# Kernel optimization log

Hardware: AMD Instinct MI355X
Metric: run time of the kernel (lower is better)

## Reference

```python
import jax, jax.numpy as jnp
import numpy as np

ALPHA = 0.2  # LeakyReLU negative slope (init arg `alpha`)
N, F_IN, F_OUT = 8192, 512, 256


def setup_inputs() -> dict:
    key = jax.random.key(0)
    k1, k2, k3, k4 = jax.random.split(key, 4)
    x = jax.random.normal(k1, (N, F_IN), dtype=jnp.float32)
    adj = jax.random.randint(k2, (N, N), 0, 2, dtype=jnp.int32)
    W = jax.random.normal(k3, (F_IN, F_OUT), dtype=jnp.float32) * (1.0 / np.sqrt(F_IN))
    a = jax.random.normal(k4, (2 * F_OUT, 1), dtype=jnp.float32) * (1.0 / np.sqrt(F_IN))
    return {"x": x, "adj": adj, "W": W, "a": a}


def reference(x, adj, W, a):
    h = x @ W  # [N, F_OUT]
    f_out = W.shape[1]
    # e[i,j] = LeakyReLU(a1 . h_i + a2 . h_j); computed without the O(N^2*2F) concat
    f1 = h @ a[:f_out, 0]   # [N]
    f2 = h @ a[f_out:, 0]   # [N]
    s = f1[:, None] + f2[None, :]  # [N, N]
    e = jnp.where(s >= 0, s, ALPHA * s)
    # Faithful to the source bug: -9e15 * zeros_like == zeros, so masked entries are 0.0
    att = jnp.where(adj > 0, e, jnp.zeros((), dtype=e.dtype))
    att = jax.nn.softmax(att, axis=1)
    # dropout is identity in eval mode
    h_prime = att @ h  # [N, F_OUT]
    return jax.nn.elu(h_prime)  # concat=True branch
```

## Files before the change

### kernel.cpp

```cpp
#include <hip/hip_runtime.h>
#include <stdint.h>

#define NN 8192
#define FIN 512
#define FOUT 256
#define ALPHA 0.2f
#define KSPLIT 4
#define KSLICE (NN / KSPLIT)
#define BK 32

typedef float f32x4 __attribute__((ext_vector_type(4)));
typedef short s16x8 __attribute__((ext_vector_type(8)));
typedef short s16x4 __attribute__((ext_vector_type(4)));

__device__ __forceinline__ uint16_t f2bf(float f) {
  union { float f; uint32_t u; } v; v.f = f;
  uint32_t u = v.u + 0x7fffu + ((v.u >> 16) & 1u);
  return (uint16_t)(u >> 16);
}

__global__ __launch_bounds__(256) void k_wa(const float* __restrict__ W,
                                            const float* __restrict__ a,
                                            float* __restrict__ wa1, float* __restrict__ wa2) {
  __shared__ float a1[256], a2[256];
  int tid = threadIdx.x;
  a1[tid] = a[tid];
  a2[tid] = a[tid + 256];
  __syncthreads();
  int m = blockIdx.x * 256 + tid;
  const float* wrow = W + (size_t)m * FOUT;
  float s1 = 0.f, s2 = 0.f;
  for (int k = 0; k < FOUT; k += 4) {
    f32x4 v = *(const f32x4*)(wrow + k);
#pragma unroll
    for (int i = 0; i < 4; i++) {
      s1 += v[i] * a1[k + i];
      s2 += v[i] * a2[k + i];
    }
  }
  wa1[m] = s1; wa2[m] = s2;
}

__global__ __launch_bounds__(256) void k_f1f2(const float* __restrict__ x,
                                              const float* __restrict__ wa1,
                                              const float* __restrict__ wa2,
                                              float* __restrict__ f1, float* __restrict__ f2) {
  __shared__ float s1[512], s2[512];
  int tid = threadIdx.x;
  s1[tid] = wa1[tid]; s1[tid + 256] = wa1[tid + 256];
  s2[tid] = wa2[tid]; s2[tid + 256] = wa2[tid + 256];
  __syncthreads();
  int w = tid >> 6, l = tid & 63;
  int row = blockIdx.x * 4 + w;
  const float* xr = x + (size_t)row * FIN + l * 8;
  f32x4 v0 = *(const f32x4*)xr;
  f32x4 v1 = *(const f32x4*)(xr + 4);
  int kb = l * 8;
  float d1 = 0.f, d2 = 0.f;
#pragma unroll
  for (int i = 0; i < 4; i++) {
    d1 += v0[i] * s1[kb + i] + v1[i] * s1[kb + 4 + i];
    d2 += v0[i] * s2[kb + i] + v1[i] * s2[kb + 4 + i];
  }
#pragma unroll
  for (int off = 32; off; off >>= 1) {
    d1 += __shfl_down(d1, off);
    d2 += __shfl_down(d2, off);
  }
  if (l == 0) { f1[row] = d1; f2[row] = d2; }
}

__global__ __launch_bounds__(256) void k_prep_wt(const float* __restrict__ W,
                                                 uint16_t* __restrict__ wt) {
  int idx = blockIdx.x * 256 + threadIdx.x;
  int f  = idx >> 7;
  int k4 = (idx & 127) * 4;
  ushort4 o;
  o.x = f2bf(W[(size_t)(k4 + 0) * FOUT + f]);
  o.y = f2bf(W[(size_t)(k4 + 1) * FOUT + f]);
  o.z = f2bf(W[(size_t)(k4 + 2) * FOUT + f]);
  o.w = f2bf(W[(size_t)(k4 + 3) * FOUT + f]);
  *(ushort4*)(wt + (size_t)f * FIN + k4) = o;
}

__global__ __launch_bounds__(512, 4) void k_gemm_h(const float* __restrict__ x,
                                                   const uint16_t* __restrict__ wt,
                                                   uint16_t* __restrict__ ht) {
  __shared__ __align__(16) uint16_t Xs[64][40];
  __shared__ __align__(16) uint16_t Ws[256][40];
  int i0 = blockIdx.x * 64;
  int tid = threadIdx.x;
  int l = tid & 63, w = tid >> 6;
  int q = l >> 4, r16 = l & 15;
  f32x4 acc[4][2];
#pragma unroll
  for (int a = 0; a < 4; a++)
#pragma unroll
    for (int b = 0; b < 2; b++) acc[a][b] = (f32x4)0.f;

  int xr = tid >> 3, xc = (tid & 7) * 4;
  int wr = tid >> 1, wc = (tid & 1) * 16;
  const float* xp = x + (size_t)(i0 + xr) * FIN + xc;
  const uint16_t* wp = wt + (size_t)wr * FIN + wc;

  f32x4 xv = *(const f32x4*)xp;
  uint4 wA = *(const uint4*)wp;
  uint4 wB = *(const uint4*)(wp + 8);

  const int ITERS = FIN / BK;
  for (int s = 0; s < ITERS; s++) {
    int sn = (s + 1 < ITERS) ? (s + 1) : s;
    f32x4 xv2 = *(const f32x4*)(xp + sn * BK);
    uint4 wA2 = *(const uint4*)(wp + sn * BK);
    uint4 wB2 = *(const uint4*)(wp + sn * BK + 8);

    s16x4 xb;
#pragma unroll
    for (int i = 0; i < 4; i++) xb[i] = (short)f2bf(xv[i]);
    *(s16x4*)(&Xs[xr][xc]) = xb;
    *(uint4*)(&Ws[wr][wc]) = wA;
    *(uint4*)(&Ws[wr][wc + 8]) = wB;
    __syncthreads();

    s16x8 Af[4], Bf[2];
#pragma unroll
    for (int a = 0; a < 4; a++) Af[a] = *(const s16x8*)(&Xs[a * 16 + r16][q * 8]);
#pragma unroll
    for (int b = 0; b < 2; b++) Bf[b] = *(const s16x8*)(&Ws[w * 32 + b * 16 + r16][q * 8]);
#pragma unroll
    for (int a = 0; a < 4; a++)
#pragma unroll
      for (int b = 0; b < 2; b++)
        acc[a][b] = __builtin_amdgcn_mfma_f32_16x16x32_bf16(Af[a], Bf[b], acc[a][b], 0, 0, 0);
    __syncthreads();
    xv = xv2; wA = wA2; wB = wB2;
  }

#pragma unroll
  for (int a = 0; a < 4; a++)
#pragma unroll
    for (int b = 0; b < 2; b++) {
      int f = w * 32 + b * 16 + r16;
      int i = i0 + a * 16 + q * 4;
      ushort4 o;
      o.x = f2bf(acc[a][b][0]); o.y = f2bf(acc[a][b][1]);
      o.z = f2bf(acc[a][b][2]); o.w = f2bf(acc[a][b][3]);
      *(ushort4*)(ht + (size_t)f * NN + i) = o;
    }
}

__global__ __launch_bounds__(256) void k_zero(float* __restrict__ l_arr) {
  l_arr[blockIdx.x * 256 + threadIdx.x] = 0.f;
}

__global__ __launch_bounds__(512, 4) void k_att(const int* __restrict__ adj,
                                                const uint16_t* __restrict__ ht,
                                                const float* __restrict__ f1,
                                                const float* __restrict__ f2,
                                                float* __restrict__ l_arr,
                                                float* __restrict__ part) {
  __shared__ __align__(16) uint16_t Ps[64][40];
  __shared__ __align__(16) uint16_t Hs[256][40];
  __shared__ __align__(16) float Fs[KSLICE];
  int i0 = blockIdx.x * 64;
  int jbase = blockIdx.y * KSLICE;
  int tid = threadIdx.x;
  int l = tid & 63, w = tid >> 6;
  int q = l >> 4, r16 = l & 15;
  int pr = tid >> 3, pc = tid & 7;
  int hr = tid >> 1, hc = (tid & 1) * 16;

  *(f32x4*)(&Fs[tid * 4]) = *(const f32x4*)(f2 + jbase + tid * 4);

  float f1i = f1[i0 + pr];
  float lsum = 0.f;
  f32x4 acc[4][2];
#pragma unroll
  for (int a = 0; a < 4; a++)
#pragma unroll
    for (int b = 0; b < 2; b++) acc[a][b] = (f32x4)0.f;

  const int* adjp = adj + (size_t)(i0 + pr) * NN + jbase + pc * 4;
  const uint16_t* htp = ht + (size_t)hr * NN + jbase + hc;

  int4 adjR = *(const int4*)adjp;
  uint4 hA = *(const uint4*)htp;
  uint4 hB = *(const uint4*)(htp + 8);
  __syncthreads();

  const int ITERS = KSLICE / BK;
  for (int s = 0; s < ITERS; s++) {
    int sn = (s + 1 < ITERS) ? (s + 1) : s;
    int4 adjN = *(const int4*)(adjp + (size_t)sn * BK);
    uint4 hA2 = *(const uint4*)(htp + sn * BK);
    uint4 hB2 = *(const uint4*)(htp + sn * BK + 8);

    f32x4 F = *(const f32x4*)(&Fs[s * BK + pc * 4]);
    s16x4 pv;
#pragma unroll
    for (int i = 0; i < 4; i++) {
      float s_ = f1i + F[i];
      float e_ = fmaxf(s_, ALPHA * s_);
      int av = (i == 0) ? adjR.x : (i == 1) ? adjR.y : (i == 2) ? adjR.z : adjR.w;
      float p_ = (av != 0) ? __expf(e_) : 1.0f;
      lsum += p_;
      pv[i] = (short)f2bf(p_);
    }
    *(s16x4*)(&Ps[pr][pc * 4]) = pv;
    *(uint4*)(&Hs[hr][hc]) = hA;
    *(uint4*)(&Hs[hr][hc + 8]) = hB;
    __syncthreads();

    s16x8 Af[4], Bf[2];
#pragma unroll
    for (int a = 0; a < 4; a++) Af[a] = *(const s16x8*)(&Ps[a * 16 + r16][q * 8]);
#pragma unroll
    for (int b = 0; b < 2; b++) Bf[b] = *(const s16x8*)(&Hs[w * 32 + b * 16 + r16][q * 8]);
#pragma unroll
    for (int a = 0; a < 4; a++)
#pragma unroll
      for (int b = 0; b < 2; b++)
        acc[a][b] = __builtin_amdgcn_mfma_f32_16x16x32_bf16(Af[a], Bf[b], acc[a][b], 0, 0, 0);
    __syncthreads();
    adjR = adjN; hA = hA2; hB = hB2;
  }

  lsum += __shfl_down(lsum, 4);
  lsum += __shfl_down(lsum, 2);
  lsum += __shfl_down(lsum, 1);
  if (pc == 0) atomicAdd(&l_arr[i0 + pr], lsum);

  float* pb = part + (size_t)blockIdx.y * ((size_t)NN * FOUT);
#pragma unroll
  for (int a = 0; a < 4; a++)
#pragma unroll
    for (int b = 0; b < 2; b++)
#pragma unroll
      for (int reg = 0; reg < 4; reg++) {
        int row = i0 + a * 16 + q * 4 + reg;
        int col = w * 32 + b * 16 + r16;
        pb[(size_t)row * FOUT + col] = acc[a][b][reg];
      }
}

__global__ __launch_bounds__(256) void k_combine(const float* __restrict__ part,
                                                 const float* __restrict__ l_arr,
                                                 float* __restrict__ out) {
  int idx = (blockIdx.x * 256 + threadIdx.x) * 4;
  float r = 1.0f / l_arr[idx >> 8];
  f32x4 v0 = *(const f32x4*)(part + 0 * (size_t)(NN * FOUT) + idx);
  f32x4 v1 = *(const f32x4*)(part + 1 * (size_t)(NN * FOUT) + idx);
  f32x4 v2 = *(const f32x4*)(part + 2 * (size_t)(NN * FOUT) + idx);
  f32x4 v3 = *(const f32x4*)(part + 3 * (size_t)(NN * FOUT) + idx);
  f32x4 o;
#pragma unroll
  for (int i = 0; i < 4; i++) {
    float v = (v0[i] + v1[i] + v2[i] + v3[i]) * r;
    o[i] = v > 0.f ? v : (__expf(v) - 1.f);
  }
  *(f32x4*)(out + idx) = o;
}

extern "C" void kernel_launch(void* const* d_in, const int* in_sizes, int n_in,
                              void* d_out, int out_size, void* d_ws, size_t ws_size,
                              hipStream_t stream) {
  const float* x   = (const float*)d_in[0];
  const int*   adj = (const int*)d_in[1];
  const float* W   = (const float*)d_in[2];
  const float* a   = (const float*)d_in[3];
  float* out = (float*)d_out;

  char* ws = (char*)d_ws;
  float*    wa1   = (float*)ws;
  float*    wa2   = wa1 + 512;
  float*    f1    = wa2 + 512;
  float*    f2    = f1 + NN;
  float*    l_arr = f2 + NN;
  uint16_t* wt    = (uint16_t*)(l_arr + NN);
  uint16_t* ht    = wt + (size_t)FOUT * FIN;
  float*    part  = (float*)(ht + (size_t)NN * FOUT);

  k_wa<<<2, 256, 0, stream>>>(W, a, wa1, wa2);
  k_f1f2<<<NN / 4, 256, 0, stream>>>(x, wa1, wa2, f1, f2);
  k_prep_wt<<<128, 256, 0, stream>>>(W, wt);
  k_gemm_h<<<128, 512, 0, stream>>>(x, wt, ht);
  k_zero<<<NN / 256, 256, 0, stream>>>(l_arr);
  k_att<<<dim3(NN / 64, KSPLIT), 512, 0, stream>>>(adj, ht, f1, f2, l_arr, part);
  k_combine<<<NN * FOUT / 1024, 256, 0, stream>>>(part, l_arr, out);
}
```

Baseline: 473.6 us.

## Double-buffer attention GEMM, widen per-wave tile, raise K-split, transpose partials

The attention kernel now uses 256 threads, each wave covering 64 output columns, with a two-stage LDS double buffer and register prefetch two tiles ahead, removing one barrier per iteration. The K-split doubles to 8, partials are stored column-major with vector stores, and combine sums eight partials and scatters to row-major output. The projection GEMM is split across two column blocks with smaller workgroups. This trades extra partial-buffer traffic, uncoalesced combine stores and higher register pressure for better latency hiding and more blocks.

```diff
diff --git a/kernel.cpp b/kernel.cpp
--- a/kernel.cpp
+++ b/kernel.cpp
@@ -5,18 +5,22 @@
 #define FIN 512
 #define FOUT 256
 #define ALPHA 0.2f
-#define KSPLIT 4
+#define KSPLIT 8
 #define KSLICE (NN / KSPLIT)
 #define BK 32
+#define ITERS (KSLICE / BK)
 
 typedef float f32x4 __attribute__((ext_vector_type(4)));
 typedef short s16x8 __attribute__((ext_vector_type(8)));
-typedef short s16x4 __attribute__((ext_vector_type(4)));
 
 __device__ __forceinline__ uint16_t f2bf(float f) {
   union { float f; uint32_t u; } v; v.f = f;
   uint32_t u = v.u + 0x7fffu + ((v.u >> 16) & 1u);
   return (uint16_t)(u >> 16);
+}
+
+__device__ __forceinline__ void lds_barrier() {
+  asm volatile("s_waitcnt lgkmcnt(0)\n\ts_barrier" ::: "memory");
 }
 
 __global__ __launch_bounds__(256) void k_wa(const float* __restrict__ W,
@@ -83,12 +87,13 @@
   *(ushort4*)(wt + (size_t)f * FIN + k4) = o;
 }
 
-__global__ __launch_bounds__(512, 4) void k_gemm_h(const float* __restrict__ x,
+__global__ __launch_bounds__(256, 2) void k_gemm_h(const float* __restrict__ x,
                                                    const uint16_t* __restrict__ wt,
                                                    uint16_t* __restrict__ ht) {
   __shared__ __align__(16) uint16_t Xs[64][40];
-  __shared__ __align__(16) uint16_t Ws[256][40];
+  __shared__ __align__(16) uint16_t Ws[128][40];
   int i0 = blockIdx.x * 64;
+  int f0 = blockIdx.y * 128;
   int tid = threadIdx.x;
   int l = tid & 63, w = tid >> 6;
   int q = l >> 4, r16 = l & 15;
@@ -98,29 +103,33 @@
 #pragma unroll
     for (int b = 0; b < 2; b++) acc[a][b] = (f32x4)0.f;
 
-  int xr = tid >> 3, xc = (tid & 7) * 4;
+  int xr = tid >> 2, xc = (tid & 3) * 8;
   int wr = tid >> 1, wc = (tid & 1) * 16;
   const float* xp = x + (size_t)(i0 + xr) * FIN + xc;
-  const uint16_t* wp = wt + (size_t)wr * FIN + wc;
-
-  f32x4 xv = *(const f32x4*)xp;
+  const uint16_t* wp = wt + (size_t)(f0 + wr) * FIN + wc;
+
+  f32x4 u0 = *(const f32x4*)xp;
+  f32x4 u1 = *(const f32x4*)(xp + 4);
   uint4 wA = *(const uint4*)wp;
   uint4 wB = *(const uint4*)(wp + 8);
 
-  const int ITERS = FIN / BK;
-  for (int s = 0; s < ITERS; s++) {
-    int sn = (s + 1 < ITERS) ? (s + 1) : s;
-    f32x4 xv2 = *(const f32x4*)(xp + sn * BK);
-    uint4 wA2 = *(const uint4*)(wp + sn * BK);
-    uint4 wB2 = *(const uint4*)(wp + sn * BK + 8);
-
-    s16x4 xb;
-#pragma unroll
-    for (int i = 0; i < 4; i++) xb[i] = (short)f2bf(xv[i]);
-    *(s16x4*)(&Xs[xr][xc]) = xb;
+  const int GI = FIN / BK;
+  for (int s = 0; s < GI; s++) {
+    int sn = (s + 1 < GI) ? (s + 1) : s;
+    f32x4 u0n = *(const f32x4*)(xp + sn * BK);
+    f32x4 u1n = *(const f32x4*)(xp + sn * BK + 4);
+    uint4 wAn = *(const uint4*)(wp + sn * BK);
+    uint4 wBn = *(const uint4*)(wp + sn * BK + 8);
+
+    uint4 pk;
+    pk.x = (uint32_t)f2bf(u0[0]) | ((uint32_t)f2bf(u0[1]) << 16);
+    pk.y = (uint32_t)f2bf(u0[2]) | ((uint32_t)f2bf(u0[3]) << 16);
+    pk.z = (uint32_t)f2bf(u1[0]) | ((uint32_t)f2bf(u1[1]) << 16);
+    pk.w = (uint32_t)f2bf(u1[2]) | ((uint32_t)f2bf(u1[3]) << 16);
+    *(uint4*)(&Xs[xr][xc]) = pk;
     *(uint4*)(&Ws[wr][wc]) = wA;
     *(uint4*)(&Ws[wr][wc + 8]) = wB;
-    __syncthreads();
+    lds_barrier();
 
     s16x8 Af[4], Bf[2];
 #pragma unroll
@@ -132,15 +141,15 @@
 #pragma unroll
       for (int b = 0; b < 2; b++)
         acc[a][b] = __builtin_amdgcn_mfma_f32_16x16x32_bf16(Af[a], Bf[b], acc[a][b], 0, 0, 0);
-    __syncthreads();
-    xv = xv2; wA = wA2; wB = wB2;
+    lds_barrier();
+    u0 = u0n; u1 = u1n; wA = wAn; wB = wBn;
   }
 
 #pragma unroll
   for (int a = 0; a < 4; a++)
 #pragma unroll
     for (int b = 0; b < 2; b++) {
-      int f = w * 32 + b * 16 + r16;
+      int f = f0 + w * 32 + b * 16 + r16;
       int i = i0 + a * 16 + q * 4;
       ushort4 o;
       o.x = f2bf(acc[a][b][0]); o.y = f2bf(acc[a][b][1]);
@@ -153,79 +162,99 @@
   l_arr[blockIdx.x * 256 + threadIdx.x] = 0.f;
 }
 
-__global__ __launch_bounds__(512, 4) void k_att(const int* __restrict__ adj,
+__global__ __launch_bounds__(256, 2) void k_att(const int* __restrict__ adj,
                                                 const uint16_t* __restrict__ ht,
                                                 const float* __restrict__ f1,
                                                 const float* __restrict__ f2,
                                                 float* __restrict__ l_arr,
                                                 float* __restrict__ part) {
-  __shared__ __align__(16) uint16_t Ps[64][40];
-  __shared__ __align__(16) uint16_t Hs[256][40];
+  __shared__ __align__(16) uint16_t Ps[2][64][40];
+  __shared__ __align__(16) uint16_t Hs[2][256][40];
   __shared__ __align__(16) float Fs[KSLICE];
-  int i0 = blockIdx.x * 64;
-  int jbase = blockIdx.y * KSLICE;
-  int tid = threadIdx.x;
-  int l = tid & 63, w = tid >> 6;
-  int q = l >> 4, r16 = l & 15;
-  int pr = tid >> 3, pc = tid & 7;
-  int hr = tid >> 1, hc = (tid & 1) * 16;
+  const int i0 = blockIdx.x * 64;
+  const int jbase = blockIdx.y * KSLICE;
+  const int tid = threadIdx.x;
+  const int l = tid & 63, w = tid >> 6;
+  const int q = l >> 4, r16 = l & 15;
+  const int pr = tid >> 2, pc = tid & 3;
 
   *(f32x4*)(&Fs[tid * 4]) = *(const f32x4*)(f2 + jbase + tid * 4);
 
-  float f1i = f1[i0 + pr];
+  const float f1i = f1[i0 + pr];
   float lsum = 0.f;
-  f32x4 acc[4][2];
+  f32x4 acc[4][4];
 #pragma unroll
   for (int a = 0; a < 4; a++)
 #pragma unroll
-    for (int b = 0; b < 2; b++) acc[a][b] = (f32x4)0.f;
-
-  const int* adjp = adj + (size_t)(i0 + pr) * NN + jbase + pc * 4;
-  const uint16_t* htp = ht + (size_t)hr * NN + jbase + hc;
-
-  int4 adjR = *(const int4*)adjp;
-  uint4 hA = *(const uint4*)htp;
-  uint4 hB = *(const uint4*)(htp + 8);
-  __syncthreads();
-
-  const int ITERS = KSLICE / BK;
+    for (int b = 0; b < 4; b++) acc[a][b] = (f32x4)0.f;
+
+  const int* adjp = adj + (size_t)(i0 + pr) * NN + jbase + pc * 8;
+  const uint16_t* htp = ht + (size_t)tid * NN + jbase;
+
+  int4 adjR[2][2];
+  uint4 hR[2][4];
+
+#define LOADT(t, p) do {                                      \
+    const int* ap_ = adjp + (t) * BK;                         \
+    adjR[p][0] = *(const int4*)ap_;                           \
+    adjR[p][1] = *(const int4*)(ap_ + 4);                     \
+    const uint16_t* hp_ = htp + (t) * BK;                     \
+    hR[p][0] = *(const uint4*)(hp_);                          \
+    hR[p][1] = *(const uint4*)(hp_ + 8);                      \
+    hR[p][2] = *(const uint4*)(hp_ + 16);                     \
+    hR[p][3] = *(const uint4*)(hp_ + 24);                     \
+  } while (0)
+
+#define STAGET(t, p, bf) do {                                 \
+    f32x4 F0_ = *(const f32x4*)(&Fs[(t) * BK + pc * 8]);      \
+    f32x4 F1_ = *(const f32x4*)(&Fs[(t) * BK + pc * 8 + 4]);  \
+    s16x8 pv_;                                                \
+    const int* av_ = (const int*)&adjR[p][0];                 \
+    _Pragma("unroll")                                         \
+    for (int i_ = 0; i_ < 8; i_++) {                          \
+      float fj_ = (i_ < 4) ? F0_[i_] : F1_[i_ - 4];           \
+      float s_ = f1i + fj_;                                   \
+      float e_ = fmaxf(s_, ALPHA * s_);                       \
+      float p_ = (av_[i_] != 0) ? __expf(e_) : 1.0f;          \
+      lsum += p_;                                             \
+      pv_[i_] = (short)f2bf(p_);                              \
+    }                                                         \
+    *(s16x8*)(&Ps[bf][pr][pc * 8]) = pv_;                     \
+    *(uint4*)(&Hs[bf][tid][0])  = hR[p][0];                   \
+    *(uint4*)(&Hs[bf][tid][8])  = hR[p][1];                   \
+    *(uint4*)(&Hs[bf][tid][16]) = hR[p][2];                   \
+    *(uint4*)(&Hs[bf][tid][24]) = hR[p][3];                   \
+  } while (0)
+
+  lds_barrier();
+  LOADT(0, 0);
+  STAGET(0, 0, 0);
+  LOADT(1, 1);
+  lds_barrier();
+
   for (int s = 0; s < ITERS; s++) {
-    int sn = (s + 1 < ITERS) ? (s + 1) : s;
-    int4 adjN = *(const int4*)(adjp + (size_t)sn * BK);
-    uint4 hA2 = *(const uint4*)(htp + sn * BK);
-    uint4 hB2 = *(const uint4*)(htp + sn * BK + 8);
-
-    f32x4 F = *(const f32x4*)(&Fs[s * BK + pc * 4]);
-    s16x4 pv;
-#pragma unroll
-    for (int i = 0; i < 4; i++) {
-      float s_ = f1i + F[i];
-      float e_ = fmaxf(s_, ALPHA * s_);
-      int av = (i == 0) ? adjR.x : (i == 1) ? adjR.y : (i == 2) ? adjR.z : adjR.w;
-      float p_ = (av != 0) ? __expf(e_) : 1.0f;
-      lsum += p_;
-      pv[i] = (short)f2bf(p_);
+    int par = s & 1;
+    if (s + 2 < ITERS) LOADT(s + 2, par);
+
+    s16x8 Af[4], Bf[4];
+#pragma unroll
+    for (int a = 0; a < 4; a++) Af[a] = *(const s16x8*)(&Ps[par][a * 16 + r16][q * 8]);
+#pragma unroll
+    for (int b = 0; b < 4; b++) Bf[b] = *(const s16x8*)(&Hs[par][w * 64 + b * 16 + r16][q * 8]);
+#pragma unroll
+    for (int a = 0; a < 4; a++)
+#pragma unroll
+      for (int b = 0; b < 4; b++)
+        acc[a][b] = __builtin_amdgcn_mfma_f32_16x16x32_bf16(Af[a], Bf[b], acc[a][b], 0, 0, 0);
+
+    if (s + 1 < ITERS) {
+      STAGET(s + 1, (s + 1) & 1, (s + 1) & 1);
+      lds_barrier();
     }
-    *(s16x4*)(&Ps[pr][pc * 4]) = pv;
-    *(uint4*)(&Hs[hr][hc]) = hA;
-    *(uint4*)(&Hs[hr][hc + 8]) = hB;
-    __syncthreads();
-
-    s16x8 Af[4], Bf[2];
-#pragma unroll
-    for (int a = 0; a < 4; a++) Af[a] = *(const s16x8*)(&Ps[a * 16 + r16][q * 8]);
-#pragma unroll
-    for (int b = 0; b < 2; b++) Bf[b] = *(const s16x8*)(&Hs[w * 32 + b * 16 + r16][q * 8]);
-#pragma unroll
-    for (int a = 0; a < 4; a++)
-#pragma unroll
-      for (int b = 0; b < 2; b++)
-        acc[a][b] = __builtin_amdgcn_mfma_f32_16x16x32_bf16(Af[a], Bf[b], acc[a][b], 0, 0, 0);
-    __syncthreads();
-    adjR = adjN; hA = hA2; hB = hB2;
-  }
-
-  lsum += __shfl_down(lsum, 4);
+  }
+#undef LOADT
+#undef STAGET
+
   lsum += __shfl_down(lsum, 2);
   lsum += __shfl_down(lsum, 1);
   if (pc == 0) atomicAdd(&l_arr[i0 + pr], lsum);
@@ -234,31 +263,31 @@
 #pragma unroll
   for (int a = 0; a < 4; a++)
 #pragma unroll
-    for (int b = 0; b < 2; b++)
-#pragma unroll
-      for (int reg = 0; reg < 4; reg++) {
-        int row = i0 + a * 16 + q * 4 + reg;
-        int col = w * 32 + b * 16 + r16;
-        pb[(size_t)row * FOUT + col] = acc[a][b][reg];
-      }
+    for (int b = 0; b < 4; b++) {
+      int col = w * 64 + b * 16 + r16;
+      int row0 = i0 + a * 16 + q * 4;
+      *(f32x4*)(pb + (size_t)col * NN + row0) = acc[a][b];
+    }
 }
 
 __global__ __launch_bounds__(256) void k_combine(const float* __restrict__ part,
                                                  const float* __restrict__ l_arr,
                                                  float* __restrict__ out) {
-  int idx = (blockIdx.x * 256 + threadIdx.x) * 4;
-  float r = 1.0f / l_arr[idx >> 8];
-  f32x4 v0 = *(const f32x4*)(part + 0 * (size_t)(NN * FOUT) + idx);
-  f32x4 v1 = *(const f32x4*)(part + 1 * (size_t)(NN * FOUT) + idx);
-  f32x4 v2 = *(const f32x4*)(part + 2 * (size_t)(NN * FOUT) + idx);
-  f32x4 v3 = *(const f32x4*)(part + 3 * (size_t)(NN * FOUT) + idx);
-  f32x4 o;
+  int t = blockIdx.x * 256 + threadIdx.x;
+  int base = t * 4;
+  int col = base >> 13;
+  int row0 = base & (NN - 1);
+  f32x4 sum = (f32x4)0.f;
+#pragma unroll
+  for (int p = 0; p < KSPLIT; p++)
+    sum += *(const f32x4*)(part + (size_t)p * NN * FOUT + base);
+  f32x4 lv = *(const f32x4*)(l_arr + row0);
 #pragma unroll
   for (int i = 0; i < 4; i++) {
-    float v = (v0[i] + v1[i] + v2[i] + v3[i]) * r;
-    o[i] = v > 0.f ? v : (__expf(v) - 1.f);
-  }
-  *(f32x4*)(out + idx) = o;
+    float v = sum[i] / lv[i];
+    float e = v > 0.f ? v : (__expf(v) - 1.f);
+    out[(size_t)(row0 + i) * FOUT + col] = e;
+  }
 }
 
 extern "C" void kernel_launch(void* const* d_in, const int* in_sizes, int n_in,
@@ -281,10 +310,10 @@
   float*    part  = (float*)(ht + (size_t)NN * FOUT);
 
   k_wa<<<2, 256, 0, stream>>>(W, a, wa1, wa2);
+  k_prep_wt<<<128, 256, 0, stream>>>(W, wt);
   k_f1f2<<<NN / 4, 256, 0, stream>>>(x, wa1, wa2, f1, f2);
-  k_prep_wt<<<128, 256, 0, stream>>>(W, wt);
-  k_gemm_h<<<128, 512, 0, stream>>>(x, wt, ht);
   k_zero<<<NN / 256, 256, 0, stream>>>(l_arr);
-  k_att<<<dim3(NN / 64, KSPLIT), 512, 0, stream>>>(adj, ht, f1, f2, l_arr, part);
+  k_gemm_h<<<dim3(128, 2), 256, 0, stream>>>(x, wt, ht);
+  k_att<<<dim3(NN / 64, KSPLIT), 256, 0, stream>>>(adj, ht, f1, f2, l_arr, part);
   k_combine<<<NN * FOUT / 1024, 256, 0, stream>>>(part, l_arr, out);
 }
```

After: 649.4 us. 37.1% more time.
